# Performance work log

Hardware: AMD Instinct MI355X
Metric: run time of the kernel (lower is better)

The kernel has to match this reference:

```python
import jax, jax.numpy as jnp
import numpy as np

B, S, D, H = 4, 2048, 768, 12
HD = D // H

def rope_cos_sin(seq_len, head_dim, dtype=jnp.float32):
    inv_freq = 1.0 / (10000.0 ** (jnp.arange(0, head_dim, 2, dtype=jnp.float32) / head_dim))
    ang = jnp.arange(seq_len, dtype=jnp.float32)[:, None] * inv_freq[None, :]  # (S, HD/2)
    cos = jnp.concatenate([jnp.cos(ang), jnp.cos(ang)], axis=-1).astype(dtype)  # (S, HD)
    sin = jnp.concatenate([jnp.sin(ang), jnp.sin(ang)], axis=-1).astype(dtype)
    return cos, sin

def rotate_half(x):
    x1, x2 = jnp.split(x, 2, axis=-1)
    return jnp.concatenate([-x2, x1], axis=-1)

def setup_inputs() -> dict:
    key = jax.random.key(0)
    k0, k1, k2, k3, k4 = jax.random.split(key, 5)
    s = 0.02
    return {
        "embeds": jax.random.normal(k0, (B, S, D), jnp.float32),
        "Wq": jax.random.normal(k1, (D, D), jnp.float32) * s,
        "Wk": jax.random.normal(k2, (D, D), jnp.float32) * s,
        "Wv": jax.random.normal(k3, (D, D), jnp.float32) * s,
        "Wo": jax.random.normal(k4, (D, D), jnp.float32) * s,
        "bo": jnp.zeros((D,), jnp.float32),
    }

def reference(embeds, Wq, Wk, Wv, Wo, bo):
    b, n, d = embeds.shape
    scale = 1.0 / np.sqrt(HD)
    # projections (torch Linear: x @ W.T), reshape to (b, H, n, HD)
    def proj(W):
        return (embeds @ W.T).reshape(b, n, H, HD).transpose(0, 2, 1, 3)
    q, k, v = proj(Wq), proj(Wk), proj(Wv)
    cos, sin = rope_cos_sin(n, HD)  # (n, HD)
    cos, sin = cos[None, None], sin[None, None]
    q = q * cos + rotate_half(q) * sin
    k = k * cos + rotate_half(k) * sin
    scores = jnp.einsum('bhqd,bhkd->bhqk', q, k)
    causal = jnp.triu(jnp.ones((n, n), bool), k=1)
    scores = jnp.where(causal, -jnp.inf, scores) * scale
    attn = jax.nn.softmax(scores, axis=-1)
    ctx = jnp.einsum('bhqk,bhkd->bhqd', attn, v)
    ctx = ctx.transpose(0, 2, 1, 3).reshape(b, n, d)
    return ctx @ Wo.T + bo
```

## Files before the change

kernel.cpp:

```cpp
#include <hip/hip_runtime.h>
#include <hip/hip_bf16.h>

using bf16x8 = __attribute__((ext_vector_type(8))) short;
using f32x4  = __attribute__((ext_vector_type(4))) float;

#define DEVI __device__ __forceinline__

static constexpr int S_LEN = 2048, D_MODEL = 768, NH = 12, HDIM = 64;
static constexpr float QSCALE = 0.125f * 1.4426950408889634f;

DEVI unsigned short f2bf(float x) {
    unsigned u = __builtin_bit_cast(unsigned, x);
    u += 0x7fffu + ((u >> 16) & 1u);
    return (unsigned short)(u >> 16);
}

DEVI unsigned short bf16c(float x) {
    return __builtin_bit_cast(unsigned short, __float2bfloat16(x));
}

#define GLL16(gsrc, ldst) __builtin_amdgcn_global_load_lds( \
    (const __attribute__((address_space(1))) void*)(gsrc),  \
    (__attribute__((address_space(3))) void*)(ldst), 16, 0, 0)

DEVI bf16x8 lds_frag(const unsigned short* lds, int row, int cb) {
    return *(const bf16x8*)((const char*)lds + row * 128 + (cb ^ ((row & 7) << 4)));
}

__global__ __launch_bounds__(256) void prep_kernel(
        const float* __restrict__ emb, const float* __restrict__ Wq, const float* __restrict__ Wk,
        const float* __restrict__ Wv, const float* __restrict__ Wo,
        unsigned short* __restrict__ emb_bf, unsigned short* __restrict__ wq_bf,
        unsigned short* __restrict__ wk_bf, unsigned short* __restrict__ wv_bf,
        unsigned short* __restrict__ wo_bf, float* __restrict__ cos_t, float* __restrict__ sin_t) {
    constexpr int NE4 = 1572864;
    constexpr int NW4 = 147456;
    constexpr int EMB_BLOCKS = NE4 / 256;
    constexpr int W_BLOCKS   = 4 * NW4 / 256;
    int bx = blockIdx.x;
    if (bx < EMB_BLOCKS) {
        int i = bx * 256 + threadIdx.x;
        float4 v = reinterpret_cast<const float4*>(emb)[i];
        ushort4 o; o.x = f2bf(v.x); o.y = f2bf(v.y); o.z = f2bf(v.z); o.w = f2bf(v.w);
        reinterpret_cast<ushort4*>(emb_bf)[i] = o;
    } else if (bx < EMB_BLOCKS + W_BLOCKS) {
        int i = (bx - EMB_BLOCKS) * 256 + threadIdx.x;
        int m = i / NW4, off = i - m * NW4;
        const float* s = (m == 0) ? Wq : (m == 1) ? Wk : (m == 2) ? Wv : Wo;
        unsigned short* d = (m == 0) ? wq_bf : (m == 1) ? wk_bf : (m == 2) ? wv_bf : wo_bf;
        float4 v = reinterpret_cast<const float4*>(s)[off];
        ushort4 o; o.x = f2bf(v.x); o.y = f2bf(v.y); o.z = f2bf(v.z); o.w = f2bf(v.w);
        reinterpret_cast<ushort4*>(d)[off] = o;
    } else {
        int idx = (bx - EMB_BLOCKS - W_BLOCKS) * 256 + threadIdx.x;
        int s = idx >> 5, f = idx & 31;
        float inv = exp2f(-(float)f * (13.287712379549449f / 32.0f));
        float ang = (float)s * inv;
        cos_t[idx] = cosf(ang);
        sin_t[idx] = sinf(ang);
    }
}

DEVI void stage128x64(const unsigned short* __restrict__ g, unsigned short* lds,
                      int ldg, int row0, int k0, int wave, int lane) {
    int rl = lane >> 3;
    int cb = (lane & 7) << 4;
    #pragma unroll
    for (int i = 0; i < 4; ++i) {
        int r = wave * 32 + i * 8 + rl;
        const char* src = (const char*)(g + (size_t)(row0 + r) * ldg + k0) + (cb ^ ((r & 7) << 4));
        GLL16(src, lds + (wave * 32 + i * 8) * 64);
    }
}

DEVI void gemm_core(const unsigned short* __restrict__ Ag, const unsigned short* __restrict__ Bg,
                    int m0, int n0, int K, int lda, int ldb,
                    unsigned short* As, unsigned short* Bs, f32x4 acc[4][4]) {
    int tid = threadIdx.x, wave = tid >> 6, lane = tid & 63;
    int wr = wave >> 1, wc = wave & 1, lrow = lane & 15, lk = lane >> 4;
    #pragma unroll
    for (int mi = 0; mi < 4; ++mi)
        #pragma unroll
        for (int ni = 0; ni < 4; ++ni) acc[mi][ni] = f32x4{0.f, 0.f, 0.f, 0.f};
    for (int k0 = 0; k0 < K; k0 += 64) {
        stage128x64(Ag, As, lda, m0, k0, wave, lane);
        stage128x64(Bg, Bs, ldb, n0, k0, wave, lane);
        __syncthreads();
        #pragma unroll
        for (int kk = 0; kk < 2; ++kk) {
            bf16x8 a[4], b[4];
            #pragma unroll
            for (int mi = 0; mi < 4; ++mi) a[mi] = lds_frag(As, wr * 64 + mi * 16 + lrow, kk * 64 + lk * 16);
            #pragma unroll
            for (int ni = 0; ni < 4; ++ni) b[ni] = lds_frag(Bs, wc * 64 + ni * 16 + lrow, kk * 64 + lk * 16);
            __builtin_amdgcn_s_setprio(1);
            #pragma unroll
            for (int mi = 0; mi < 4; ++mi)
                #pragma unroll
                for (int ni = 0; ni < 4; ++ni)
                    acc[mi][ni] = __builtin_amdgcn_mfma_f32_16x16x32_bf16(a[mi], b[ni], acc[mi][ni], 0, 0, 0);
            __builtin_amdgcn_s_setprio(0);
        }
        __syncthreads();
    }
}

__global__ __launch_bounds__(256) void qkv_kernel(
        const unsigned short* __restrict__ Xg,
        const unsigned short* __restrict__ Wqg, const unsigned short* __restrict__ Wkg,
        const unsigned short* __restrict__ Wvg,
        const float* __restrict__ cos_t, const float* __restrict__ sin_t,
        unsigned short* __restrict__ Qo, unsigned short* __restrict__ Ko,
        unsigned short* __restrict__ Vt) {
    __shared__ unsigned short sbuf[128 * 128];
    unsigned short* As = sbuf;
    unsigned short* Bs = sbuf + 128 * 64;
    int z = blockIdx.z;
    const unsigned short* Wg = (z == 0) ? Wqg : ((z == 1) ? Wkg : Wvg);
    int m0 = blockIdx.x * 128, n0 = blockIdx.y * 128;
    f32x4 acc[4][4];
    gemm_core(Xg, Wg, m0, n0, D_MODEL, D_MODEL, D_MODEL, As, Bs, acc);

    int tid = threadIdx.x, wave = tid >> 6, lane = tid & 63;
    int wr = wave >> 1, wc = wave & 1, lrow = lane & 15, lk = lane >> 4;

    if (z < 2) {
        unsigned short* O = (z == 0) ? Qo : Ko;
        float qs = (z == 0) ? QSCALE : 1.0f;
        int h = blockIdx.y * 2 + wc;
        #pragma unroll
        for (int mi = 0; mi < 4; ++mi) {
            #pragma unroll
            for (int r = 0; r < 4; ++r) {
                int m = m0 + wr * 64 + mi * 16 + lk * 4 + r;
                int bb = m >> 11, spos = m & 2047;
                size_t base = ((size_t)(bb * NH + h) * S_LEN + spos) * HDIM;
                #pragma unroll
                for (int nf = 0; nf < 2; ++nf) {
                    int hd = nf * 16 + lrow;
                    float c = cos_t[spos * 32 + hd], sn = sin_t[spos * 32 + hd];
                    float x1 = acc[mi][nf][r], x2 = acc[mi][nf + 2][r];
                    O[base + hd]      = f2bf((x1 * c - x2 * sn) * qs);
                    O[base + hd + 32] = f2bf((x2 * c + x1 * sn) * qs);
                }
            }
        }
    } else {
        unsigned short* T = sbuf;
        #pragma unroll
        for (int mi = 0; mi < 4; ++mi)
            #pragma unroll
            for (int nt = 0; nt < 4; ++nt) {
                int hd  = wc * 64 + nt * 16 + lrow;
                int sp0 = wr * 64 + mi * 16 + lk * 4;
                ushort4 pk;
                pk.x = f2bf(acc[mi][nt][0]); pk.y = f2bf(acc[mi][nt][1]);
                pk.z = f2bf(acc[mi][nt][2]); pk.w = f2bf(acc[mi][nt][3]);
                *(ushort4*)((char*)T + ((hd * 256 + sp0 * 2) ^ ((hd & 7) << 4))) = pk;
            }
        __syncthreads();
        int hd = tid >> 1, half = tid & 1;
        int h  = blockIdx.y * 2 + (hd >> 6), hdh = hd & 63;
        int bb = m0 >> 11, sp_abs = (m0 & 2047) + half * 64;
        unsigned short* dst = Vt + ((size_t)(bb * NH + h) * HDIM + hdh) * S_LEN + sp_abs;
        #pragma unroll
        for (int j = 0; j < 8; ++j) {
            bf16x8 v = *(const bf16x8*)((const char*)T +
                        ((hd * 256 + half * 128 + j * 16) ^ ((hd & 7) << 4)));
            *(bf16x8*)((char*)dst + j * 16) = v;
        }
    }
}

DEVI void attn_stage(const unsigned short* __restrict__ Kb, const unsigned short* __restrict__ Vt,
                     unsigned short* Ksb, unsigned short* Vsb,
                     int bh, int kv0, int wave, int lane) {
    int rl = lane >> 3, cb = (lane & 7) << 4;
    #pragma unroll
    for (int i = 0; i < 2; ++i) {
        int r = wave * 16 + i * 8 + rl;
        int scb = cb ^ ((r & 7) << 4);
        const char* srck = (const char*)(Kb + ((size_t)bh * S_LEN + kv0 + r) * HDIM) + scb;
        GLL16(srck, Ksb + (wave * 16 + i * 8) * 64);
        const char* srcv = (const char*)(Vt + ((size_t)bh * HDIM + r) * S_LEN + kv0) + scb;
        GLL16(srcv, Vsb + (wave * 16 + i * 8) * 64);
    }
}

DEVI void do_qkt_sw(const bf16x8 (&kf)[2][4], bf16x8 qf0, bf16x8 qf1, f32x4 (&sc)[4]) {
    #pragma unroll
    for (int nt = 0; nt < 4; ++nt) sc[nt] = f32x4{0.f, 0.f, 0.f, 0.f};
    __builtin_amdgcn_s_setprio(1);
    #pragma unroll
    for (int kk = 0; kk < 2; ++kk) {
        bf16x8 qf = kk ? qf1 : qf0;
        #pragma unroll
        for (int nt = 0; nt < 4; ++nt)
            sc[nt] = __builtin_amdgcn_mfma_f32_16x16x32_bf16(kf[kk][nt], qf, sc[nt], 0, 0, 0);
    }
    __builtin_amdgcn_s_setprio(0);
}

template <bool DIAG>
DEVI void do_softmax_sw(const f32x4 (&sc)[4], unsigned short* Pw, f32x4 o[4],
                        float& mrow, float& lsum, int lrow, int lk, int qrel) {
    float t[16];
    #pragma unroll
    for (int nt = 0; nt < 4; ++nt)
        #pragma unroll
        for (int r = 0; r < 4; ++r) {
            float v = sc[nt][r];
            if (DIAG && (nt * 16 + lk * 4 + r > qrel)) v = -__builtin_inff();
            t[nt * 4 + r] = v;
        }
    float mx = fmaxf(fmaxf(t[0], t[1]), t[2]);
    mx = fmaxf(fmaxf(mx, t[3]), t[4]);
    mx = fmaxf(fmaxf(mx, t[5]), t[6]);
    mx = fmaxf(fmaxf(mx, t[7]), t[8]);
    mx = fmaxf(fmaxf(mx, t[9]), t[10]);
    mx = fmaxf(fmaxf(mx, t[11]), t[12]);
    mx = fmaxf(fmaxf(mx, t[13]), t[14]);
    mx = fmaxf(mx, t[15]);
    mx = fmaxf(mx, __shfl_xor(mx, 16, 64));
    mx = fmaxf(mx, __shfl_xor(mx, 32, 64));
    if (!__all(mx <= mrow + 8.0f)) {
        float mnew = fmaxf(mrow, mx);
        float alpha = exp2f(mrow - mnew);
        mrow = mnew;
        lsum *= alpha;
        #pragma unroll
        for (int nt = 0; nt < 4; ++nt) o[nt] *= alpha;
    }
    float ps = 0.f;
    #pragma unroll
    for (int nt = 0; nt < 4; ++nt) {
        float p0 = exp2f(t[nt * 4 + 0] - mrow), p1 = exp2f(t[nt * 4 + 1] - mrow);
        float p2 = exp2f(t[nt * 4 + 2] - mrow), p3 = exp2f(t[nt * 4 + 3] - mrow);
        ps += (p0 + p1) + (p2 + p3);
        ushort4 pk;
        pk.x = bf16c(p0); pk.y = bf16c(p1); pk.z = bf16c(p2); pk.w = bf16c(p3);
        *(ushort4*)((char*)Pw + lrow * 128 + (((nt * 16 + lk * 4) * 2) ^ ((lrow & 7) << 4))) = pk;
    }
    ps += __shfl_xor(ps, 16, 64);
    ps += __shfl_xor(ps, 32, 64);
    lsum += ps;
}

DEVI void do_pv_sw(const bf16x8 (&vf)[2][4], const unsigned short* Pw, f32x4 o[4],
                   int lrow, int lk) {
    __builtin_amdgcn_s_setprio(1);
    #pragma unroll
    for (int kk = 0; kk < 2; ++kk) {
        bf16x8 pf = lds_frag(Pw, lrow, kk * 64 + lk * 16);
        #pragma unroll
        for (int nt = 0; nt < 4; ++nt)
            o[nt] = __builtin_amdgcn_mfma_f32_16x16x32_bf16(vf[kk][nt], pf, o[nt], 0, 0, 0);
    }
    __builtin_amdgcn_s_setprio(0);
}

DEVI void attn_epilogue(const f32x4 o[4], float lsum, int qt, int bh,
                        unsigned short* __restrict__ Ctx, int lrow, int lk, int wave) {
    float inv = 1.0f / lsum;
    int b = bh / NH, h = bh % NH;
    int spos = qt * 64 + wave * 16 + lrow;
    size_t base = ((size_t)(b * S_LEN + spos)) * D_MODEL + h * HDIM;
    #pragma unroll
    for (int nt = 0; nt < 4; ++nt) {
        ushort4 pk;
        pk.x = bf16c(o[nt][0] * inv); pk.y = bf16c(o[nt][1] * inv);
        pk.z = bf16c(o[nt][2] * inv); pk.w = bf16c(o[nt][3] * inv);
        *(ushort4*)(Ctx + base + nt * 16 + lk * 4) = pk;
    }
}

__global__ __launch_bounds__(256, 3) void attn_kernel(
        const unsigned short* __restrict__ Q, const unsigned short* __restrict__ Kb,
        const unsigned short* __restrict__ Vt, unsigned short* __restrict__ Ctx) {
    __shared__ unsigned short Ks[2][64 * 64], Vs[2][64 * 64], Ps[4][16 * 64];
    int id = blockIdx.x;
    int n  = (id & 7) * 96 + (id >> 3);
    int bh = n >> 4;
    int pj = n & 15;
    int qa = pj, qb = 31 - pj;
    int tid = threadIdx.x, wave = tid >> 6, lane = tid & 63;
    int lrow = lane & 15, lk = lane >> 4;
    int qrel = wave * 16 + lrow;

    const unsigned short* qpa = Q + ((size_t)bh * S_LEN + qa * 64 + qrel) * HDIM;
    const unsigned short* qpb = Q + ((size_t)bh * S_LEN + qb * 64 + qrel) * HDIM;
    bf16x8 qfa0 = *(const bf16x8*)(qpa + lk * 8);
    bf16x8 qfa1 = *(const bf16x8*)(qpa + 32 + lk * 8);
    bf16x8 qfb0 = *(const bf16x8*)(qpb + lk * 8);
    bf16x8 qfb1 = *(const bf16x8*)(qpb + 32 + lk * 8);

    f32x4 oa[4], ob[4];
    float ma = -__builtin_inff(), la = 0.f, mb = -__builtin_inff(), lb = 0.f;
    #pragma unroll
    for (int nt = 0; nt < 4; ++nt) { oa[nt] = f32x4{0.f, 0.f, 0.f, 0.f}; ob[nt] = f32x4{0.f, 0.f, 0.f, 0.f}; }

    attn_stage(Kb, Vt, Ks[0], Vs[0], bh, 0, wave, lane);
    int cur = 0;
    f32x4 sc[4];
    for (int kt = 0; kt <= qb; ++kt) {
        __syncthreads();
        if (kt < qb) attn_stage(Kb, Vt, Ks[cur ^ 1], Vs[cur ^ 1], bh, (kt + 1) * 64, wave, lane);

        bf16x8 kf[2][4], vf[2][4];
        #pragma unroll
        for (int kk = 0; kk < 2; ++kk)
            #pragma unroll
            for (int nt = 0; nt < 4; ++nt) {
                kf[kk][nt] = lds_frag(Ks[cur], nt * 16 + lrow, kk * 64 + lk * 16);
                vf[kk][nt] = lds_frag(Vs[cur], nt * 16 + lrow, kk * 64 + lk * 16);
            }

        if (kt <= qa) {
            do_qkt_sw(kf, qfa0, qfa1, sc);
            if (kt == qa) do_softmax_sw<true >(sc, Ps[wave], oa, ma, la, lrow, lk, qrel);
            else          do_softmax_sw<false>(sc, Ps[wave], oa, ma, la, lrow, lk, qrel);
            do_pv_sw(vf, Ps[wave], oa, lrow, lk);
        }
        do_qkt_sw(kf, qfb0, qfb1, sc);
        if (kt == qb) do_softmax_sw<true >(sc, Ps[wave], ob, mb, lb, lrow, lk, qrel);
        else          do_softmax_sw<false>(sc, Ps[wave], ob, mb, lb, lrow, lk, qrel);
        do_pv_sw(vf, Ps[wave], ob, lrow, lk);
        cur ^= 1;
    }

    attn_epilogue(oa, la, qa, bh, Ctx, lrow, lk, wave);
    attn_epilogue(ob, lb, qb, bh, Ctx, lrow, lk, wave);
}

__global__ __launch_bounds__(256) void outproj_kernel(
        const unsigned short* __restrict__ Cg, const unsigned short* __restrict__ Wog,
        const float* __restrict__ bo, float* __restrict__ Out) {
    __shared__ unsigned short As[128 * 64], Bs[128 * 64];
    int m0 = blockIdx.x * 128, n0 = blockIdx.y * 128;
    f32x4 acc[4][4];
    gemm_core(Cg, Wog, m0, n0, D_MODEL, D_MODEL, D_MODEL, As, Bs, acc);

    int tid = threadIdx.x, wave = tid >> 6, lane = tid & 63;
    int wr = wave >> 1, wc = wave & 1, lrow = lane & 15, lk = lane >> 4;
    #pragma unroll
    for (int mi = 0; mi < 4; ++mi)
        #pragma unroll
        for (int r = 0; r < 4; ++r) {
            int m = m0 + wr * 64 + mi * 16 + lk * 4 + r;
            #pragma unroll
            for (int nt = 0; nt < 4; ++nt) {
                int n = n0 + wc * 64 + nt * 16 + lrow;
                Out[(size_t)m * D_MODEL + n] = acc[mi][nt][r] + bo[n];
            }
        }
}

extern "C" void kernel_launch(void* const* d_in, const int* in_sizes, int n_in,
                              void* d_out, int out_size, void* d_ws, size_t ws_size,
                              hipStream_t stream) {
    const float* embeds = (const float*)d_in[0];
    const float* Wq = (const float*)d_in[1];
    const float* Wk = (const float*)d_in[2];
    const float* Wv = (const float*)d_in[3];
    const float* Wo = (const float*)d_in[4];
    const float* bo = (const float*)d_in[5];
    float* out = (float*)d_out;

    const size_t NE = (size_t)4 * 2048 * 768;
    const size_t NW = (size_t)768 * 768;

    unsigned short* ws     = (unsigned short*)d_ws;
    unsigned short* emb_bf = ws;
    unsigned short* wq_bf  = emb_bf + NE;
    unsigned short* wk_bf  = wq_bf + NW;
    unsigned short* wv_bf  = wk_bf + NW;
    unsigned short* wo_bf  = wv_bf + NW;
    unsigned short* qb     = wo_bf + NW;
    unsigned short* kb     = qb + NE;
    unsigned short* vt     = kb + NE;
    float* cos_t = (float*)(vt + NE);
    float* sin_t = cos_t + 2048 * 32;
    unsigned short* ctx = emb_bf;

    prep_kernel<<<dim3(8704), 256, 0, stream>>>(embeds, Wq, Wk, Wv, Wo,
                                                emb_bf, wq_bf, wk_bf, wv_bf, wo_bf,
                                                cos_t, sin_t);
    qkv_kernel<<<dim3(64, 6, 3), 256, 0, stream>>>(emb_bf, wq_bf, wk_bf, wv_bf,
                                                   cos_t, sin_t, qb, kb, vt);
    attn_kernel<<<dim3(768), 256, 0, stream>>>(qb, kb, vt, ctx);
    outproj_kernel<<<dim3(64, 6), 256, 0, stream>>>(ctx, wo_bf, bo, out);
}
```

Measured before the change: 151.2 us.

## Transpose RoPE tables for vector loads and load V fragments just-in-time

The RoPE cos/sin tables are now stored head-dim-major (hd*2048+spos), so the QK projection epilogue can fetch four consecutive sequence positions with one float4 load instead of scalar gathers. In the attention loop, V fragments are no longer preloaded into registers with the K fragments. They are read from LDS inside each PV MFMA step, which lowers register pressure and may raise occupancy. The cost is that V is read from LDS twice per tile (once per query block) instead of once.

```diff
diff --git a/kernel.cpp b/kernel.cpp
--- a/kernel.cpp
+++ b/kernel.cpp
@@ -53,9 +53,9 @@
         reinterpret_cast<ushort4*>(d)[off] = o;
     } else {
         int idx = (bx - EMB_BLOCKS - W_BLOCKS) * 256 + threadIdx.x;
-        int s = idx >> 5, f = idx & 31;
-        float inv = exp2f(-(float)f * (13.287712379549449f / 32.0f));
-        float ang = (float)s * inv;
+        int hd = idx >> 11, spos = idx & 2047;
+        float inv = exp2f(-(float)hd * (13.287712379549449f / 32.0f));
+        float ang = (float)spos * inv;
         cos_t[idx] = cosf(ang);
         sin_t[idx] = sinf(ang);
     }
@@ -130,18 +130,20 @@
         int h = blockIdx.y * 2 + wc;
         #pragma unroll
         for (int mi = 0; mi < 4; ++mi) {
-            #pragma unroll
-            for (int r = 0; r < 4; ++r) {
-                int m = m0 + wr * 64 + mi * 16 + lk * 4 + r;
-                int bb = m >> 11, spos = m & 2047;
-                size_t base = ((size_t)(bb * NH + h) * S_LEN + spos) * HDIM;
+            int m_base = m0 + wr * 64 + mi * 16 + lk * 4;
+            int bb = m_base >> 11, sp0 = m_base & 2047;
+            size_t obase = ((size_t)(bb * NH + h) * S_LEN + sp0) * HDIM;
+            #pragma unroll
+            for (int nf = 0; nf < 2; ++nf) {
+                int hd = nf * 16 + lrow;
+                float4 c4 = *(const float4*)(cos_t + hd * 2048 + sp0);
+                float4 s4 = *(const float4*)(sin_t + hd * 2048 + sp0);
                 #pragma unroll
-                for (int nf = 0; nf < 2; ++nf) {
-                    int hd = nf * 16 + lrow;
-                    float c = cos_t[spos * 32 + hd], sn = sin_t[spos * 32 + hd];
+                for (int r = 0; r < 4; ++r) {
+                    float c = ((const float*)&c4)[r], sn = ((const float*)&s4)[r];
                     float x1 = acc[mi][nf][r], x2 = acc[mi][nf + 2][r];
-                    O[base + hd]      = f2bf((x1 * c - x2 * sn) * qs);
-                    O[base + hd + 32] = f2bf((x2 * c + x1 * sn) * qs);
+                    O[obase + (size_t)r * HDIM + hd]      = f2bf((x1 * c - x2 * sn) * qs);
+                    O[obase + (size_t)r * HDIM + hd + 32] = f2bf((x2 * c + x1 * sn) * qs);
                 }
             }
         }
@@ -246,15 +248,17 @@
     lsum += ps;
 }
 
-DEVI void do_pv_sw(const bf16x8 (&vf)[2][4], const unsigned short* Pw, f32x4 o[4],
+DEVI void do_pv_sw(const unsigned short* Vs, const unsigned short* Pw, f32x4 o[4],
                    int lrow, int lk) {
     __builtin_amdgcn_s_setprio(1);
     #pragma unroll
     for (int kk = 0; kk < 2; ++kk) {
         bf16x8 pf = lds_frag(Pw, lrow, kk * 64 + lk * 16);
         #pragma unroll
-        for (int nt = 0; nt < 4; ++nt)
-            o[nt] = __builtin_amdgcn_mfma_f32_16x16x32_bf16(vf[kk][nt], pf, o[nt], 0, 0, 0);
+        for (int nt = 0; nt < 4; ++nt) {
+            bf16x8 vf = lds_frag(Vs, nt * 16 + lrow, kk * 64 + lk * 16);
+            o[nt] = __builtin_amdgcn_mfma_f32_16x16x32_bf16(vf, pf, o[nt], 0, 0, 0);
+        }
     }
     __builtin_amdgcn_s_setprio(0);
 }
@@ -306,25 +310,23 @@
         __syncthreads();
         if (kt < qb) attn_stage(Kb, Vt, Ks[cur ^ 1], Vs[cur ^ 1], bh, (kt + 1) * 64, wave, lane);
 
-        bf16x8 kf[2][4], vf[2][4];
+        bf16x8 kf[2][4];
         #pragma unroll
         for (int kk = 0; kk < 2; ++kk)
             #pragma unroll
-            for (int nt = 0; nt < 4; ++nt) {
+            for (int nt = 0; nt < 4; ++nt)
                 kf[kk][nt] = lds_frag(Ks[cur], nt * 16 + lrow, kk * 64 + lk * 16);
-                vf[kk][nt] = lds_frag(Vs[cur], nt * 16 + lrow, kk * 64 + lk * 16);
-            }
 
         if (kt <= qa) {
             do_qkt_sw(kf, qfa0, qfa1, sc);
             if (kt == qa) do_softmax_sw<true >(sc, Ps[wave], oa, ma, la, lrow, lk, qrel);
             else          do_softmax_sw<false>(sc, Ps[wave], oa, ma, la, lrow, lk, qrel);
-            do_pv_sw(vf, Ps[wave], oa, lrow, lk);
+            do_pv_sw(Vs[cur], Ps[wave], oa, lrow, lk);
         }
         do_qkt_sw(kf, qfb0, qfb1, sc);
         if (kt == qb) do_softmax_sw<true >(sc, Ps[wave], ob, mb, lb, lrow, lk, qrel);
         else          do_softmax_sw<false>(sc, Ps[wave], ob, mb, lb, lrow, lk, qrel);
-        do_pv_sw(vf, Ps[wave], ob, lrow, lk);
+        do_pv_sw(Vs[cur], Ps[wave], ob, lrow, lk);
         cur ^= 1;
     }
 
```

After: 150.3 us. No clear change (-0.6%).
